# Optimization experiments

Measured on AMD Instinct MI355X. Metric: run time of the kernel, lower is better.

The kernel has to match this reference:

```python
import jax, jax.numpy as jnp
import numpy as np

QUERY_DIM = 192
KEY_DIM = 64
DIM_OUT = 128
C = QUERY_DIM + KEY_DIM  # 256
N = 10000
E = 320000
M = 5000


def setup_inputs() -> dict:
    key = jax.random.key(0)
    ks = jax.random.split(key, 16)
    s = 1.0 / np.sqrt(C)
    inp = {
        "query": jax.random.normal(ks[0], (N, QUERY_DIM), jnp.float32),
        "key_idx": jax.random.randint(ks[1], (N,), 0, KEY_DIM),
        "edge_index": jax.random.randint(ks[2], (2, E), 0, N),
        "mask_idx": jnp.sort(jax.random.randint(ks[3], (M,), 0, N)),
        "Wq": jax.random.normal(ks[4], (C, C), jnp.float32) * s,
        "bq": jnp.zeros((C,), jnp.float32),
        "Wk": jax.random.normal(ks[5], (C, C), jnp.float32) * s,
        "bk": jnp.zeros((C,), jnp.float32),
        "Wv": jax.random.normal(ks[6], (C, C), jnp.float32) * s,
        "bv": jnp.zeros((C,), jnp.float32),
        "Ws": jax.random.normal(ks[7], (C, C), jnp.float32) * s,
        "bs": jnp.zeros((C,), jnp.float32),
        "Wo": jax.random.normal(ks[8], (KEY_DIM, DIM_OUT), jnp.float32) * (1.0 / np.sqrt(KEY_DIM)),
        "bo": jnp.zeros((DIM_OUT,), jnp.float32),
    }
    return inp


def reference(query, key_idx, edge_index, mask_idx, Wq, bq, Wk, bk, Wv, bv, Ws, bs, Wo, bo):
    # node features: [N, C] = concat(query, one_hot(key))
    x = jnp.concatenate([query, jax.nn.one_hot(key_idx, KEY_DIM, dtype=query.dtype)], axis=1)
    src, dst = edge_index[0], edge_index[1]  # messages flow src -> dst
    # node-level projections (dense GEMMs), then edge gather
    q_n = x @ Wq + bq
    k_n = x @ Wk + bk
    v_n = x @ Wv + bv
    q = q_n[dst]  # [E, C]
    k = k_n[src]
    v = v_n[src]
    score = jnp.sum(q * k, axis=-1) / jnp.sqrt(jnp.asarray(C, x.dtype))  # [E]
    # per-destination softmax over incoming edges
    m = jax.ops.segment_max(score, dst, num_segments=N)  # [N]
    m = jnp.where(jnp.isfinite(m), m, 0.0)
    e = jnp.exp(score - m[dst])
    denom = jax.ops.segment_sum(e, dst, num_segments=N)
    alpha = e / (denom[dst] + 1e-16)
    # scatter-aggregate weighted values + root/skip connection
    agg = jax.ops.segment_sum(alpha[:, None] * v, dst, num_segments=N)  # [N, C]
    out = agg + (x @ Ws + bs)
    h = jax.nn.relu(out[mask_idx])  # [M, C]
    h = h[:, QUERY_DIM:]  # [M, KEY_DIM]
    return h @ Wo + bo  # [M, DIM_OUT]
```

## Files before the change

### kernel.cpp

```cpp
#include <hip/hip_runtime.h>

#define QDIM 192
#define KDIM 64
#define CDIM 256
#define DOUT 128
#define CAPS 64
#define NVCOL 640
#define NEG_INF __int_as_float(0xFF800000)

typedef _Float16 hf2 __attribute__((ext_vector_type(2)));
typedef _Float16 half4 __attribute__((ext_vector_type(4)));
typedef _Float16 half8 __attribute__((ext_vector_type(8)));
typedef float floatx4 __attribute__((ext_vector_type(4)));

#if defined(__has_builtin)
#if __has_builtin(__builtin_amdgcn_fdot2)
#define HAVE_FDOT2 1
#endif
#endif

__device__ __forceinline__ hf2 bc_h2(unsigned u) { return __builtin_bit_cast(hf2, u); }

__device__ __forceinline__ float dot2acc(hf2 a, hf2 b, float c) {
#ifdef HAVE_FDOT2
    return __builtin_amdgcn_fdot2(a, b, c, false);
#else
    return c + (float)a[0] * (float)b[0] + (float)a[1] * (float)b[1];
#endif
}

__global__ __launch_bounds__(256) void prep_kernel(
        const float* __restrict__ query, _Float16* __restrict__ Qh,
        const float* __restrict__ Wq, const float* __restrict__ bq,
        const float* __restrict__ Wk, const float* __restrict__ bk,
        const float* __restrict__ Wv, const float* __restrict__ bv,
        const float* __restrict__ Ws, const float* __restrict__ bs,
        const int* __restrict__ mask, int M,
        _Float16* __restrict__ WhT, float* __restrict__ OB,
        int* __restrict__ deg4, int qchunks, int N) {
    int t = blockIdx.x * blockDim.x + threadIdx.x;
    if (t < qchunks) {
        float4 v = ((const float4*)query)[t];
        half4 h = { (_Float16)v.x, (_Float16)v.y, (_Float16)v.z, (_Float16)v.w };
        ((half4*)Qh)[t] = h;
        return;
    }
    t -= qchunks;
    if (t < NVCOL * QDIM) {
        int v = t / QDIM, r = t - v * QDIM;
        const float* Wseg; int col;
        if (v < 256)      { Wseg = Wq; col = v; }
        else if (v < 512) { Wseg = Wk; col = v - 256; }
        else if (v < 576) { Wseg = Wv; col = QDIM + (v - 512); }
        else              { Wseg = Ws; col = QDIM + (v - 576); }
        WhT[t] = (_Float16)Wseg[(size_t)r * CDIM + col];
        return;
    }
    t -= NVCOL * QDIM;
    if (t < NVCOL * KDIM) {
        int v = t >> 6, kidx = t & 63;
        const float* Wseg; const float* bseg; int col;
        if (v < 256)      { Wseg = Wq; bseg = bq; col = v; }
        else if (v < 512) { Wseg = Wk; bseg = bk; col = v - 256; }
        else if (v < 576) { Wseg = Wv; bseg = bv; col = QDIM + (v - 512); }
        else              { Wseg = Ws; bseg = bs; col = QDIM + (v - 576); }
        OB[t] = Wseg[(size_t)(QDIM + kidx) * CDIM + col] + bseg[col];
        return;
    }
    t -= NVCOL * KDIM;
    if (t < 4 * N) {
        int node = t >> 2;
        int lo = 0, hi = M;
        while (lo < hi) { int mid = (lo + hi) >> 1; if (mask[mid] < node) lo = mid + 1; else hi = mid; }
        bool found = (lo < M) && (mask[lo] == node);
        deg4[t] = found ? 0 : (int)0x80000000;
    }
}

__global__ __launch_bounds__(256) void gemm_nodes(
        const _Float16* __restrict__ Qh, const int* __restrict__ key_idx,
        const _Float16* __restrict__ WhT, const float* __restrict__ OB,
        const int* __restrict__ esrc, const int* __restrict__ edst,
        const int* __restrict__ mask, int M,
        int* deg4, int* __restrict__ adj, int E,
        _Float16* __restrict__ Qbuf, _Float16* __restrict__ Kbuf,
        _Float16* __restrict__ Vbuf, float* __restrict__ Sbuf, int N) {
    int tid = threadIdx.x;
    int z = blockIdx.z;
    int bm = blockIdx.x * 64;

    bool doe[2] = {false, false};
    int srcv[2]; size_t ci[2] = {0, 0};
    if (z == 0) {
        int stride = gridDim.x * gridDim.y * 256;
        int base = (blockIdx.y * gridDim.x + blockIdx.x) * 256 + tid;
        #pragma unroll
        for (int q = 0; q < 2; q++) {
            int e = base + q * stride;
            if (e < E) {
                int d = edst[e];
                size_t c = (size_t)d * 4 + (e & 3);
                if (deg4[c] >= 0) {
                    doe[q] = true; srcv[q] = esrc[e]; ci[q] = c;
                }
            }
        }
        if (bm >= N) {
            #pragma unroll
            for (int q = 0; q < 2; q++)
                if (doe[q]) { int s = atomicAdd(&deg4[ci[q]], 1); if ((unsigned)s < CAPS) adj[ci[q] * CAPS + s] = srcv[q]; }
            return;
        }
    } else {
        if (bm >= M) return;
    }

    int bn = (z == 0) ? 256 + blockIdx.y * 64
                      : (blockIdx.y < 4 ? blockIdx.y * 64 : 576);

    int w = tid >> 6, l = tid & 63;
    int lrow = l & 15, quad = l >> 4;

    int ra = w * 16 + lrow;
    int gra = (z == 0) ? min(bm + ra, N - 1) : mask[min(bm + ra, M - 1)];
    const _Float16* abase = Qh + (size_t)gra * QDIM + quad * 8;
    half8 af[6];
    #pragma unroll
    for (int ks = 0; ks < 6; ks++) af[ks] = *(const half8*)(abase + ks * 32);

    floatx4 acc[4] = {{0.f,0.f,0.f,0.f},{0.f,0.f,0.f,0.f},{0.f,0.f,0.f,0.f},{0.f,0.f,0.f,0.f}};
    #pragma unroll
    for (int nt = 0; nt < 4; nt++) {
        const _Float16* bbase = WhT + (size_t)(bn + nt * 16 + lrow) * QDIM + quad * 8;
        #pragma unroll
        for (int ks = 0; ks < 6; ks++) {
            half8 bf = *(const half8*)(bbase + ks * 32);
            acc[nt] = __builtin_amdgcn_mfma_f32_16x16x32_f16(af[ks], bf, acc[nt], 0, 0, 0);
        }
    }

    int ki[4], grs[4];
    #pragma unroll
    for (int reg = 0; reg < 4; reg++) {
        int re = w * 16 + quad * 4 + reg;
        grs[reg] = (z == 0) ? min(bm + re, N - 1) : mask[min(bm + re, M - 1)];
        ki[reg] = key_idx[grs[reg]];
    }
    #pragma unroll
    for (int nt = 0; nt < 4; nt++) {
        int gc = bn + nt * 16 + lrow;
        const float* obc = OB + (size_t)gc * KDIM;
        #pragma unroll
        for (int reg = 0; reg < 4; reg++) {
            int gr = grs[reg];
            float v = acc[nt][reg] + obc[ki[reg]];
            if (gc < 256)      Qbuf[(size_t)gr * 256 + gc] = (_Float16)v;
            else if (gc < 512) Kbuf[(size_t)gr * 256 + (gc - 256)] = (_Float16)v;
            else if (gc < 576) Vbuf[(size_t)gr * KDIM + (gc - 512)] = (_Float16)v;
            else               Sbuf[(size_t)gr * KDIM + (gc - 576)] = v;
        }
    }

    #pragma unroll
    for (int q = 0; q < 2; q++)
        if (doe[q]) { int s = atomicAdd(&deg4[ci[q]], 1); if ((unsigned)s < CAPS) adj[ci[q] * CAPS + s] = srcv[q]; }
}

__global__ __launch_bounds__(256) void attend_out(
        const _Float16* __restrict__ Qbuf, const _Float16* __restrict__ Kbuf,
        const _Float16* __restrict__ Vbuf, const float* __restrict__ Sbuf,
        const int* __restrict__ deg4, const int* __restrict__ adj,
        const int* __restrict__ mask, const float* __restrict__ Wo,
        const float* __restrict__ bo, float* __restrict__ out, int M) {
    int w = threadIdx.x >> 6, lane = threadIdx.x & 63;
    int r = blockIdx.x * 4 + w;
    if (r >= M) return;
    int node = mask[r];
    if (r > 0 && mask[r - 1] == node) return;
    int l = lane & 15, g = lane >> 4;

    const uint4* qp = (const uint4*)(Qbuf + (size_t)node * 256 + l * 16);
    uint4 qa = qp[0], qb = qp[1];
    hf2 qh[8] = { bc_h2(qa.x), bc_h2(qa.y), bc_h2(qa.z), bc_h2(qa.w),
                  bc_h2(qb.x), bc_h2(qb.y), bc_h2(qb.z), bc_h2(qb.w) };

    int dn_g = min(deg4[(size_t)node * 4 + g], CAPS);
    int d0 = __shfl(dn_g, 0, 64), d1 = __shfl(dn_g, 16, 64);
    int d2 = __shfl(dn_g, 32, 64), d3 = __shfl(dn_g, 48, 64);
    int O1 = d0, O2 = d0 + d1, O3 = d0 + d1 + d2, T = O3 + d3;
    const size_t base4 = (size_t)node * 4 * CAPS;
    auto fs = [&](int j) -> int {
        int b = (j >= O1) + (j >= O2) + (j >= O3);
        int off = j - (b == 0 ? 0 : b == 1 ? O1 : b == 2 ? O2 : O3);
        return adj[base4 + (size_t)b * CAPS + off];
    };

    float m = NEG_INF, dsum = 0.f;
    float a0 = 0.f, a1 = 0.f, a2 = 0.f, a3 = 0.f;

    uint4 ka, kb; uint2 vv; int s_nxt = 0;
    if (g < T) {
        int s0 = fs(g);
        const uint4* kp = (const uint4*)(Kbuf + (size_t)s0 * 256 + l * 16);
        ka = kp[0]; kb = kp[1];
        vv = *(const uint2*)(Vbuf + (size_t)s0 * KDIM + l * 4);
        s_nxt = (g + 4 < T) ? fs(g + 4) : s0;
    }
    for (int j = g; j < T; j += 4) {
        const uint4* kp2 = (const uint4*)(Kbuf + (size_t)s_nxt * 256 + l * 16);
        uint4 ka2 = kp2[0], kb2 = kp2[1];
        uint2 vv2 = *(const uint2*)(Vbuf + (size_t)s_nxt * KDIM + l * 4);
        int s_aft = (j + 8 < T) ? fs(j + 8) : s_nxt;

        float d = 0.f;
        d = dot2acc(bc_h2(ka.x), qh[0], d);
        d = dot2acc(bc_h2(ka.y), qh[1], d);
        d = dot2acc(bc_h2(ka.z), qh[2], d);
        d = dot2acc(bc_h2(ka.w), qh[3], d);
        d = dot2acc(bc_h2(kb.x), qh[4], d);
        d = dot2acc(bc_h2(kb.y), qh[5], d);
        d = dot2acc(bc_h2(kb.z), qh[6], d);
        d = dot2acc(bc_h2(kb.w), qh[7], d);
        d += __shfl_xor(d, 1, 64);
        d += __shfl_xor(d, 2, 64);
        d += __shfl_xor(d, 4, 64);
        d += __shfl_xor(d, 8, 64);
        float sc = d * 0.0625f;
        float m_new = fmaxf(m, sc);
        float scale = __expf(m - m_new);
        float p = __expf(sc - m_new);
        dsum = dsum * scale + p;
        hf2 v01 = bc_h2(vv.x), v23 = bc_h2(vv.y);
        a0 = a0 * scale + p * (float)v01[0];
        a1 = a1 * scale + p * (float)v01[1];
        a2 = a2 * scale + p * (float)v23[0];
        a3 = a3 * scale + p * (float)v23[1];
        m = m_new;
        ka = ka2; kb = kb2; vv = vv2; s_nxt = s_aft;
    }

    float Mx = fmaxf(m, __shfl_xor(m, 16, 64));
    Mx = fmaxf(Mx, __shfl_xor(Mx, 32, 64));
    float wgt = (m == NEG_INF) ? 0.f : __expf(m - Mx);
    float ds = dsum * wgt;
    ds += __shfl_xor(ds, 16, 64);
    ds += __shfl_xor(ds, 32, 64);
    a0 *= wgt; a1 *= wgt; a2 *= wgt; a3 *= wgt;
    a0 += __shfl_xor(a0, 16, 64); a0 += __shfl_xor(a0, 32, 64);
    a1 += __shfl_xor(a1, 16, 64); a1 += __shfl_xor(a1, 32, 64);
    a2 += __shfl_xor(a2, 16, 64); a2 += __shfl_xor(a2, 32, 64);
    a3 += __shfl_xor(a3, 16, 64); a3 += __shfl_xor(a3, 32, 64);
    float inv = 1.f / (ds + 1e-16f);

    float4 s4 = *((const float4*)(Sbuf + (size_t)node * KDIM + l * 4));
    float h0 = fmaxf(a0 * inv + s4.x, 0.f);
    float h1 = fmaxf(a1 * inv + s4.y, 0.f);
    float h2 = fmaxf(a2 * inv + s4.z, 0.f);
    float h3 = fmaxf(a3 * inv + s4.w, 0.f);

    float o0 = bo[lane], o1 = bo[lane + 64];
    #pragma unroll
    for (int c = 0; c < KDIM; c++) {
        float hc = (c & 3) == 0 ? h0 : (c & 3) == 1 ? h1 : (c & 3) == 2 ? h2 : h3;
        float hv = __shfl(hc, c >> 2, 64);
        o0 += hv * Wo[c * DOUT + lane];
        o1 += hv * Wo[c * DOUT + 64 + lane];
    }
    int rr = r;
    do {
        out[(size_t)rr * DOUT + lane] = o0;
        out[(size_t)rr * DOUT + 64 + lane] = o1;
        rr++;
    } while (rr < M && mask[rr] == node);
}

extern "C" void kernel_launch(void* const* d_in, const int* in_sizes, int n_in,
                              void* d_out, int out_size, void* d_ws, size_t ws_size,
                              hipStream_t stream) {
    const float* query    = (const float*)d_in[0];
    const int* key_idx    = (const int*)d_in[1];
    const int* edge_index = (const int*)d_in[2];
    const int* mask_idx   = (const int*)d_in[3];
    const float* Wq = (const float*)d_in[4];
    const float* bq = (const float*)d_in[5];
    const float* Wk = (const float*)d_in[6];
    const float* bk = (const float*)d_in[7];
    const float* Wv = (const float*)d_in[8];
    const float* bv = (const float*)d_in[9];
    const float* Ws = (const float*)d_in[10];
    const float* bs = (const float*)d_in[11];
    const float* Wo = (const float*)d_in[12];
    const float* bo = (const float*)d_in[13];

    int N = in_sizes[0] / QDIM;
    int E = in_sizes[2] / 2;
    int M = in_sizes[3];
    const int* esrc = edge_index;
    const int* edst = edge_index + E;

    char* wsb = (char*)d_ws;
    size_t off = 0;
    auto alloc = [&](size_t nbytes) { char* p = wsb + off; off += (nbytes + 15) & ~15ull; return p; };
    _Float16* Qh   = (_Float16*)alloc((size_t)N * QDIM * 2);
    _Float16* WhT  = (_Float16*)alloc((size_t)NVCOL * QDIM * 2);
    float* OB      = (float*)alloc((size_t)NVCOL * KDIM * 4);
    _Float16* Qbuf = (_Float16*)alloc((size_t)N * 256 * 2);
    _Float16* Kbuf = (_Float16*)alloc((size_t)N * 256 * 2);
    _Float16* Vbuf = (_Float16*)alloc((size_t)N * KDIM * 2);
    float* Sbuf    = (float*)alloc((size_t)N * KDIM * 4);
    int*   deg4    = (int*)alloc((size_t)N * 4 * 4);
    int*   adj     = (int*)alloc((size_t)N * 4 * CAPS * 4);

    int qchunks = N * QDIM / 4;
    int total1 = qchunks + NVCOL * QDIM + NVCOL * KDIM + 4 * N;
    prep_kernel<<<(total1 + 255) / 256, 256, 0, stream>>>(
        query, Qh, Wq, bq, Wk, bk, Wv, bv, Ws, bs, mask_idx, M, WhT, OB, deg4, qchunks, N);

    int xa = (N + 63) / 64, xm = (M + 63) / 64;
    dim3 ggrid((unsigned)max(xa, xm), 5, 2);
    gemm_nodes<<<ggrid, 256, 0, stream>>>(Qh, key_idx, WhT, OB, esrc, edst,
                                          mask_idx, M, deg4, adj, E,
                                          Qbuf, Kbuf, Vbuf, Sbuf, N);

    attend_out<<<(M + 3) / 4, 256, 0, stream>>>(Qbuf, Kbuf, Vbuf, Sbuf, deg4, adj,
                                                mask_idx, Wo, bo, (float*)d_out, M);
}
```

Before: 138.6 us.

## Stage weight tile in LDS, overlap edge atomics with GEMM, deepen gather prefetch

The node GEMM now copies the 64-column weight tile into padded shared memory once per block and reads B fragments from LDS instead of global memory. The edge-bucketing atomicAdd is issued before the MFMA loop so its latency overlaps the compute, and the adj store is done afterwards. The early-return path for blocks beyond N is removed, so those blocks now run the full GEMM path on clamped rows. In attend_out the K/V gather uses a two-deep double-buffered prefetch in place of the single-step one, to hide gather latency at the cost of extra registers.

```diff
diff --git a/kernel.cpp b/kernel.cpp
--- a/kernel.cpp
+++ b/kernel.cpp
@@ -7,6 +7,7 @@
 #define CAPS 64
 #define NVCOL 640
 #define NEG_INF __int_as_float(0xFF800000)
+#define LDP 200
 
 typedef _Float16 hf2 __attribute__((ext_vector_type(2)));
 typedef _Float16 half4 __attribute__((ext_vector_type(4)));
@@ -85,6 +86,7 @@
         int* deg4, int* __restrict__ adj, int E,
         _Float16* __restrict__ Qbuf, _Float16* __restrict__ Kbuf,
         _Float16* __restrict__ Vbuf, float* __restrict__ Sbuf, int N) {
+    __shared__ __align__(16) _Float16 Bs[64 * LDP];
     int tid = threadIdx.x;
     int z = blockIdx.z;
     int bm = blockIdx.x * 64;
@@ -105,12 +107,6 @@
                 }
             }
         }
-        if (bm >= N) {
-            #pragma unroll
-            for (int q = 0; q < 2; q++)
-                if (doe[q]) { int s = atomicAdd(&deg4[ci[q]], 1); if ((unsigned)s < CAPS) adj[ci[q] * CAPS + s] = srcv[q]; }
-            return;
-        }
     } else {
         if (bm >= M) return;
     }
@@ -128,16 +124,32 @@
     #pragma unroll
     for (int ks = 0; ks < 6; ks++) af[ks] = *(const half8*)(abase + ks * 32);
 
+    #pragma unroll
+    for (int it = 0; it < 6; it++) {
+        int idx = tid + it * 256;
+        int cc = idx / 24, q4 = idx % 24;
+        uint4 vb = ((const uint4*)(WhT + (size_t)(bn + cc) * QDIM))[q4];
+        *((uint4*)&Bs[cc * LDP + q4 * 8]) = vb;
+    }
+    __syncthreads();
+
+    int slot[2] = {-1, -1};
+    #pragma unroll
+    for (int q = 0; q < 2; q++) if (doe[q]) slot[q] = atomicAdd(&deg4[ci[q]], 1);
+
     floatx4 acc[4] = {{0.f,0.f,0.f,0.f},{0.f,0.f,0.f,0.f},{0.f,0.f,0.f,0.f},{0.f,0.f,0.f,0.f}};
     #pragma unroll
-    for (int nt = 0; nt < 4; nt++) {
-        const _Float16* bbase = WhT + (size_t)(bn + nt * 16 + lrow) * QDIM + quad * 8;
+    for (int ks = 0; ks < 6; ks++) {
         #pragma unroll
-        for (int ks = 0; ks < 6; ks++) {
-            half8 bf = *(const half8*)(bbase + ks * 32);
+        for (int nt = 0; nt < 4; nt++) {
+            half8 bf = *(const half8*)(&Bs[(nt * 16 + lrow) * LDP + quad * 8 + ks * 32]);
             acc[nt] = __builtin_amdgcn_mfma_f32_16x16x32_f16(af[ks], bf, acc[nt], 0, 0, 0);
         }
     }
+
+    #pragma unroll
+    for (int q = 0; q < 2; q++)
+        if (doe[q] && (unsigned)slot[q] < CAPS) adj[ci[q] * CAPS + slot[q]] = srcv[q];
 
     int ki[4], grs[4];
     #pragma unroll
@@ -160,10 +172,6 @@
             else               Sbuf[(size_t)gr * KDIM + (gc - 576)] = v;
         }
     }
-
-    #pragma unroll
-    for (int q = 0; q < 2; q++)
-        if (doe[q]) { int s = atomicAdd(&deg4[ci[q]], 1); if ((unsigned)s < CAPS) adj[ci[q] * CAPS + s] = srcv[q]; }
 }
 
 __global__ __launch_bounds__(256) void attend_out(
@@ -194,24 +202,12 @@
         int off = j - (b == 0 ? 0 : b == 1 ? O1 : b == 2 ? O2 : O3);
         return adj[base4 + (size_t)b * CAPS + off];
     };
+    auto idxAt = [&](int p) -> int { return fs(min(g + 4 * p, T - 1)); };
 
     float m = NEG_INF, dsum = 0.f;
     float a0 = 0.f, a1 = 0.f, a2 = 0.f, a3 = 0.f;
 
-    uint4 ka, kb; uint2 vv; int s_nxt = 0;
-    if (g < T) {
-        int s0 = fs(g);
-        const uint4* kp = (const uint4*)(Kbuf + (size_t)s0 * 256 + l * 16);
-        ka = kp[0]; kb = kp[1];
-        vv = *(const uint2*)(Vbuf + (size_t)s0 * KDIM + l * 4);
-        s_nxt = (g + 4 < T) ? fs(g + 4) : s0;
-    }
-    for (int j = g; j < T; j += 4) {
-        const uint4* kp2 = (const uint4*)(Kbuf + (size_t)s_nxt * 256 + l * 16);
-        uint4 ka2 = kp2[0], kb2 = kp2[1];
-        uint2 vv2 = *(const uint2*)(Vbuf + (size_t)s_nxt * KDIM + l * 4);
-        int s_aft = (j + 8 < T) ? fs(j + 8) : s_nxt;
-
+    auto compute = [&](uint4 ka, uint4 kb, uint2 vv) {
         float d = 0.f;
         d = dot2acc(bc_h2(ka.x), qh[0], d);
         d = dot2acc(bc_h2(ka.y), qh[1], d);
@@ -236,7 +232,39 @@
         a2 = a2 * scale + p * (float)v23[0];
         a3 = a3 * scale + p * (float)v23[1];
         m = m_new;
-        ka = ka2; kb = kb2; vv = vv2; s_nxt = s_aft;
+    };
+
+    int P = (g < T) ? ((T - g + 3) >> 2) : 0;
+    uint4 kaA = {}, kbA = {}; uint2 vvA = {};
+    uint4 kaB = {}, kbB = {}; uint2 vvB = {};
+    int sC = 0, sD = 0;
+    if (P > 0) {
+        int sA = idxAt(0);
+        const uint4* kp = (const uint4*)(Kbuf + (size_t)sA * 256 + l * 16);
+        kaA = kp[0]; kbA = kp[1];
+        vvA = *(const uint2*)(Vbuf + (size_t)sA * KDIM + l * 4);
+        int sB = idxAt(1);
+        const uint4* kp2 = (const uint4*)(Kbuf + (size_t)sB * 256 + l * 16);
+        kaB = kp2[0]; kbB = kp2[1];
+        vvB = *(const uint2*)(Vbuf + (size_t)sB * KDIM + l * 4);
+        sC = idxAt(2); sD = idxAt(3);
+    }
+    for (int p = 0; p < P; p += 2) {
+        compute(kaA, kbA, vvA);
+        {
+            const uint4* kp = (const uint4*)(Kbuf + (size_t)sC * 256 + l * 16);
+            kaA = kp[0]; kbA = kp[1];
+            vvA = *(const uint2*)(Vbuf + (size_t)sC * KDIM + l * 4);
+        }
+        int sC2 = idxAt(p + 4);
+        if (p + 1 < P) compute(kaB, kbB, vvB);
+        {
+            const uint4* kp = (const uint4*)(Kbuf + (size_t)sD * 256 + l * 16);
+            kaB = kp[0]; kbB = kp[1];
+            vvB = *(const uint2*)(Vbuf + (size_t)sD * KDIM + l * 4);
+        }
+        int sD2 = idxAt(p + 5);
+        sC = sC2; sD = sD2;
     }
 
     float Mx = fmaxf(m, __shfl_xor(m, 16, 64));
```

Result: faster. 131.9 us (-4.9%).
